# Kernel optimization log

Measured on AMD Instinct MI355X. Metric: run time of the kernel, lower is better.

Reference implementation:

```python
import jax, jax.numpy as jnp
import numpy as np

THRESH = 0.01  # confidence threshold on max softmax prob

def setup_inputs() -> dict:
    key = jax.random.key(0)
    ks = jax.random.split(key, 14)
    B, D, H, C = 8192, 2048, 2048, 1000
    sD = 1.0 / np.sqrt(D)
    sH = 1.0 / np.sqrt(H)
    return {
        "x":   jax.random.normal(ks[0], (B, D), jnp.float32),
        "W1":  jax.random.normal(ks[1], (D, H), jnp.float32) * sD,
        "b1":  jnp.zeros((H,), jnp.float32),
        "W2":  jax.random.normal(ks[2], (H, H), jnp.float32) * sH,
        "b2":  jnp.zeros((H,), jnp.float32),
        "W3":  jax.random.normal(ks[3], (H, H), jnp.float32) * sH,
        "b3":  jnp.zeros((H,), jnp.float32),
        "H1w": jax.random.normal(ks[4], (H, C), jnp.float32) * sH,
        "H1b": jnp.zeros((C,), jnp.float32),
        "H2w": jax.random.normal(ks[5], (H, C), jnp.float32) * sH,
        "H2b": jnp.zeros((C,), jnp.float32),
        "Fw":  jax.random.normal(ks[6], (H, C), jnp.float32) * sH,
        "Fb":  jnp.zeros((C,), jnp.float32),
    }

def _confident(logits):
    # confidence_function: max softmax probability exceeds threshold
    p = jax.nn.softmax(logits, axis=-1)
    return jnp.max(p, axis=-1) > THRESH  # [B] bool

def reference(x, W1, b1, W2, b2, W3, b3, H1w, H1b, H2w, H2b, Fw, Fb):
    # Stage 1 backbone + partial head
    h1 = jax.nn.relu(x @ W1 + b1)          # [B,H]
    p1 = h1 @ H1w + H1b                     # [B,C]
    c1 = _confident(p1)                     # exit mask stage 1
    # Stage 2 backbone + partial head
    h2 = jax.nn.relu(h1 @ W2 + b2)
    p2 = h2 @ H2w + H2b
    c2 = _confident(p2)
    # Final stage
    h3 = jax.nn.relu(h2 @ W3 + b3)
    p3 = h3 @ Fw + Fb
    # Per-sample first-exit selection == original index_select/index_copy cascade
    out = jnp.where(c1[:, None], p1, jnp.where(c2[:, None], p2, p3))
    return out
```

## Files before the change

kernel.cpp:

```cpp
#include <hip/hip_runtime.h>
#include <math.h>

typedef __bf16 bf16x8 __attribute__((ext_vector_type(8)));
typedef float f32x4 __attribute__((ext_vector_type(4)));
typedef unsigned short ushort_t;
typedef unsigned int uint_t;

__device__ __forceinline__ ushort_t f2bf(float f) {
    uint_t u = __float_as_uint(f);
    u += 0x7fff + ((u >> 16) & 1);
    return (ushort_t)(u >> 16);
}
__device__ __forceinline__ float bf2f(ushort_t h) {
    return __uint_as_float(((uint_t)h) << 16);
}

__device__ __forceinline__ size_t poff(int row, int k, int Kdim) {
    return ((((size_t)(row >> 7) * (Kdim >> 5) + (k >> 5)) * 512)
            + ((k >> 3) & 3) * 128 + (row & 127)) * 8 + (k & 7);
}

__device__ __forceinline__ void ll16(const ushort_t* g, ushort_t* l) {
    __builtin_amdgcn_global_load_lds(
        (const __attribute__((address_space(1))) unsigned int*)g,
        (__attribute__((address_space(3))) unsigned int*)l, 16, 0, 0);
}

template <int N> __device__ __forceinline__ void wait_vmcnt() {
    if constexpr (N == 0) asm volatile("s_waitcnt vmcnt(0)" ::: "memory");
    else if constexpr (N == 1) asm volatile("s_waitcnt vmcnt(1)" ::: "memory");
    else if constexpr (N == 2) asm volatile("s_waitcnt vmcnt(2)" ::: "memory");
    else if constexpr (N == 3) asm volatile("s_waitcnt vmcnt(3)" ::: "memory");
    else if constexpr (N == 4) asm volatile("s_waitcnt vmcnt(4)" ::: "memory");
    else if constexpr (N == 5) asm volatile("s_waitcnt vmcnt(5)" ::: "memory");
    else asm volatile("s_waitcnt vmcnt(6)" ::: "memory");
}
__device__ __forceinline__ void lgkm0_fence() {
    asm volatile("s_waitcnt lgkmcnt(0)" ::: "memory");
    __builtin_amdgcn_sched_barrier(0);
}

__global__ __launch_bounds__(256) void split_kernel(
    const float* __restrict__ in, ushort_t* __restrict__ hi,
    ushort_t* __restrict__ lo, int Kdim)
{
    const int i = blockIdx.x * 256 + threadIdx.x;
    const int row = i >> 8;
    const int k = (i & 255) * 8;
    const float4 v0 = *(const float4*)(in + (size_t)row * Kdim + k);
    const float4 v1 = *(const float4*)(in + (size_t)row * Kdim + k + 4);
    const float f[8] = {v0.x, v0.y, v0.z, v0.w, v1.x, v1.y, v1.z, v1.w};
    ushort_t h[8], l[8];
    #pragma unroll
    for (int j = 0; j < 8; ++j) {
        h[j] = f2bf(f[j]);
        l[j] = f2bf(f[j] - bf2f(h[j]));
    }
    const size_t o = poff(row, k, Kdim);
    *(uint4*)(hi + o) = *(const uint4*)h;
    *(uint4*)(lo + o) = *(const uint4*)l;
}

__global__ __launch_bounds__(256) void tsplit_kernel(
    const float* __restrict__ W, ushort_t* __restrict__ hi,
    ushort_t* __restrict__ lo, int K, int N, int write_lo)
{
    __shared__ float t[32][33];
    const int tx = threadIdx.x & 31;
    const int ty = threadIdx.x >> 5;
    const int nb = blockIdx.x * 32;
    const int kb = blockIdx.y * 32;
    #pragma unroll
    for (int i = 0; i < 4; ++i) {
        int k = kb + ty + i * 8;
        int n = nb + tx;
        t[ty + i * 8][tx] = (n < N) ? W[(size_t)k * N + n] : 0.f;
    }
    __syncthreads();
    #pragma unroll
    for (int i = 0; i < 4; ++i) {
        int n = nb + ty + i * 8;
        int k = kb + tx;
        float f = t[tx][ty + i * 8];
        size_t idx = poff(n, k, K);
        ushort_t h = f2bf(f);
        hi[idx] = h;
        if (write_lo) lo[idx] = f2bf(f - bf2f(h));
    }
}

__global__ __launch_bounds__(256) void gather_pack(
    const ushort_t* __restrict__ srchi, const ushort_t* __restrict__ srclo,
    ushort_t* __restrict__ dsthi, ushort_t* __restrict__ dstlo,
    const int* __restrict__ idx, const int* __restrict__ cntp, int Kdim)
{
    const int j = blockIdx.x;
    if (j >= *cntp) return;
    const int srow = idx[j];
    const int k = threadIdx.x * 8;
    const size_t so = poff(srow, k, Kdim);
    const size_t dofs = poff(j, k, Kdim);
    *(uint4*)(dsthi + dofs) = *(const uint4*)(srchi + so);
    if (srclo) *(uint4*)(dstlo + dofs) = *(const uint4*)(srclo + so);
}


template <int BN>
__global__ __launch_bounds__(512, 2) void gemm_split3(
    const ushort_t* __restrict__ Ahi, const ushort_t* __restrict__ Alo,
    const ushort_t* __restrict__ Bhi, const ushort_t* __restrict__ Blo,
    const float* __restrict__ bias,
    float* __restrict__ Cf, ushort_t* __restrict__ Chi, ushort_t* __restrict__ Clo,
    int K, int Ntrue, int ldc, int relu_flag,
    const int* __restrict__ cntp, int Mfull)
{
    static_assert(BN == 256 || BN == 128, "BN");
    constexpr int BSLAB = BN / 128;
    constexpr int NF = BN / 64;
    constexpr int SH = 2 + BSLAB;
    constexpr int T = 2 * SH;

    __shared__ __align__(16) ushort_t sAh[2][8192];
    __shared__ __align__(16) ushort_t sAl[2][8192];
    __shared__ __align__(16) ushort_t sBh[2][BSLAB * 4096];
    __shared__ __align__(16) ushort_t sBl[2][BSLAB * 4096];

    const int tid = threadIdx.x;
    const int m0 = blockIdx.y * 256;
    const int n0 = blockIdx.x * BN;
    int Meff = Mfull;
    if (cntp) Meff = *cntp;
    if (m0 >= ((Meff + 255) & ~255)) return;

    const int lane = tid & 63, wave = tid >> 6;
    const int wm = wave >> 2, wn = wave & 3;
    const int q = lane >> 4, r16 = lane & 15;
    const int wofs = wave * 512;

    const size_t bstr = (size_t)(K >> 5) * 4096;
    const ushort_t* gAh = Ahi + (size_t)(2 * blockIdx.y) * bstr + tid * 8;
    const ushort_t* gAl = Alo + (size_t)(2 * blockIdx.y) * bstr + tid * 8;
    const ushort_t* gBh = Bhi + (size_t)(BSLAB * blockIdx.x) * bstr + tid * 8;
    const ushort_t* gBl = Blo + (size_t)(BSLAB * blockIdx.x) * bstr + tid * 8;

    int aoff[8], boff[NF];
    #pragma unroll
    for (int mi = 0; mi < 8; ++mi)
        aoff[mi] = wm * 4096 + (q * 128 + mi * 16 + r16) * 8;
    #pragma unroll
    for (int nj = 0; nj < NF; ++nj) {
        const int col = wn * (NF * 16) + nj * 16 + r16;
        boff[nj] = (col >> 7) * 4096 + (q * 128 + (col & 127)) * 8;
    }

    f32x4 acc[8][NF];
    #pragma unroll
    for (int mi = 0; mi < 8; ++mi)
        #pragma unroll
        for (int nj = 0; nj < NF; ++nj) acc[mi][nj] = (f32x4)(0.f);

    const int NT = K >> 5;

    ll16(gAh, &sAh[0][wofs]);
    ll16(gAh + bstr, &sAh[0][4096 + wofs]);
    ll16(gBh, &sBh[0][wofs]);
    if constexpr (BSLAB == 2) ll16(gBh + bstr, &sBh[0][4096 + wofs]);
    ll16(gBl, &sBl[0][wofs]);
    if constexpr (BSLAB == 2) ll16(gBl + bstr, &sBl[0][4096 + wofs]);
    ll16(gAl, &sAl[0][wofs]);
    ll16(gAl + bstr, &sAl[0][4096 + wofs]);

    bf16x8 ah[8], bh[NF];
    for (int t = 0; t < NT - 1; ++t) {
        const int c = t & 1;
        const size_t ko = (size_t)(t + 1) * 4096;

        wait_vmcnt<T - SH>();
        __builtin_amdgcn_s_barrier();
        #pragma unroll
        for (int mi = 0; mi < 8; ++mi) ah[mi] = *(const bf16x8*)(&sAh[c][aoff[mi]]);
        #pragma unroll
        for (int nj = 0; nj < NF; ++nj) bh[nj] = *(const bf16x8*)(&sBh[c][boff[nj]]);
        ll16(gAh + ko, &sAh[c ^ 1][wofs]);
        ll16(gAh + bstr + ko, &sAh[c ^ 1][4096 + wofs]);
        ll16(gBh + ko, &sBh[c ^ 1][wofs]);
        if constexpr (BSLAB == 2) ll16(gBh + bstr + ko, &sBh[c ^ 1][4096 + wofs]);
        lgkm0_fence();
        __builtin_amdgcn_s_setprio(1);
        #pragma unroll
        for (int nj = 0; nj < NF; ++nj)
            #pragma unroll
            for (int mi = 0; mi < 8; ++mi)
                acc[mi][nj] = __builtin_amdgcn_mfma_f32_16x16x32_bf16(ah[mi], bh[nj], acc[mi][nj], 0, 0, 0);
        __builtin_amdgcn_s_setprio(0);

        wait_vmcnt<T - BSLAB>();
        __builtin_amdgcn_s_barrier();
        bf16x8 bl[NF];
        #pragma unroll
        for (int nj = 0; nj < NF; ++nj) bl[nj] = *(const bf16x8*)(&sBl[c][boff[nj]]);
        ll16(gBl + ko, &sBl[c ^ 1][wofs]);
        if constexpr (BSLAB == 2) ll16(gBl + bstr + ko, &sBl[c ^ 1][4096 + wofs]);
        lgkm0_fence();
        __builtin_amdgcn_s_setprio(1);
        #pragma unroll
        for (int nj = 0; nj < NF; ++nj)
            #pragma unroll
            for (int mi = 0; mi < 8; ++mi)
                acc[mi][nj] = __builtin_amdgcn_mfma_f32_16x16x32_bf16(ah[mi], bl[nj], acc[mi][nj], 0, 0, 0);
        __builtin_amdgcn_s_setprio(0);

        wait_vmcnt<T - 2>();
        __builtin_amdgcn_s_barrier();
        bf16x8 al[8];
        #pragma unroll
        for (int mi = 0; mi < 8; ++mi) al[mi] = *(const bf16x8*)(&sAl[c][aoff[mi]]);
        ll16(gAl + ko, &sAl[c ^ 1][wofs]);
        ll16(gAl + bstr + ko, &sAl[c ^ 1][4096 + wofs]);
        lgkm0_fence();
        __builtin_amdgcn_s_setprio(1);
        #pragma unroll
        for (int nj = 0; nj < NF; ++nj)
            #pragma unroll
            for (int mi = 0; mi < 8; ++mi)
                acc[mi][nj] = __builtin_amdgcn_mfma_f32_16x16x32_bf16(al[mi], bh[nj], acc[mi][nj], 0, 0, 0);
        __builtin_amdgcn_s_setprio(0);
    }

    {
        const int c = (NT - 1) & 1;
        wait_vmcnt<T - SH>();
        __builtin_amdgcn_s_barrier();
        #pragma unroll
        for (int mi = 0; mi < 8; ++mi) ah[mi] = *(const bf16x8*)(&sAh[c][aoff[mi]]);
        #pragma unroll
        for (int nj = 0; nj < NF; ++nj) bh[nj] = *(const bf16x8*)(&sBh[c][boff[nj]]);
        lgkm0_fence();
        __builtin_amdgcn_s_setprio(1);
        #pragma unroll
        for (int nj = 0; nj < NF; ++nj)
            #pragma unroll
            for (int mi = 0; mi < 8; ++mi)
                acc[mi][nj] = __builtin_amdgcn_mfma_f32_16x16x32_bf16(ah[mi], bh[nj], acc[mi][nj], 0, 0, 0);
        __builtin_amdgcn_s_setprio(0);

        wait_vmcnt<2>();
        __builtin_amdgcn_s_barrier();
        bf16x8 bl[NF];
        #pragma unroll
        for (int nj = 0; nj < NF; ++nj) bl[nj] = *(const bf16x8*)(&sBl[c][boff[nj]]);
        lgkm0_fence();
        __builtin_amdgcn_s_setprio(1);
        #pragma unroll
        for (int nj = 0; nj < NF; ++nj)
            #pragma unroll
            for (int mi = 0; mi < 8; ++mi)
                acc[mi][nj] = __builtin_amdgcn_mfma_f32_16x16x32_bf16(ah[mi], bl[nj], acc[mi][nj], 0, 0, 0);
        __builtin_amdgcn_s_setprio(0);

        wait_vmcnt<0>();
        __builtin_amdgcn_s_barrier();
        bf16x8 al[8];
        #pragma unroll
        for (int mi = 0; mi < 8; ++mi) al[mi] = *(const bf16x8*)(&sAl[c][aoff[mi]]);
        lgkm0_fence();
        __builtin_amdgcn_s_setprio(1);
        #pragma unroll
        for (int nj = 0; nj < NF; ++nj)
            #pragma unroll
            for (int mi = 0; mi < 8; ++mi)
                acc[mi][nj] = __builtin_amdgcn_mfma_f32_16x16x32_bf16(al[mi], bh[nj], acc[mi][nj], 0, 0, 0);
        __builtin_amdgcn_s_setprio(0);
    }

    #pragma unroll
    for (int mi = 0; mi < 8; ++mi) {
        #pragma unroll
        for (int nj = 0; nj < NF; ++nj) {
            const int col = n0 + wn * (NF * 16) + nj * 16 + r16;
            const int rowb = m0 + wm * 128 + mi * 16 + q * 4;
            const float bv = (col < Ntrue) ? bias[col] : 0.f;
            #pragma unroll
            for (int r = 0; r < 4; ++r) {
                float v = acc[mi][nj][r] + bv;
                if (relu_flag) v = fmaxf(v, 0.f);
                if (Cf) {
                    if (col < Ntrue) Cf[(size_t)(rowb + r) * ldc + col] = v;
                } else {
                    const size_t idx = poff(rowb + r, col, ldc);
                    ushort_t h = f2bf(v);
                    Chi[idx] = h;
                    Clo[idx] = f2bf(v - bf2f(h));
                }
            }
        }
    }
}

template <int BN>
__global__ __launch_bounds__(512, 2) void gemm_bf16k(
    const ushort_t* __restrict__ Ahi, const ushort_t* __restrict__ Bhi,
    const float* __restrict__ bias,
    float* __restrict__ Cf, ushort_t* __restrict__ Chi,
    int K, int Ntrue, int ldc, int relu_flag,
    const int* __restrict__ cntp, int Mfull)
{
    static_assert(BN == 256 || BN == 128, "BN");
    constexpr int BSLAB = BN / 128;
    constexpr int NF = BN / 64;
    constexpr int SH = 2 + BSLAB;

    __shared__ __align__(16) ushort_t sA[4][8192];
    __shared__ __align__(16) ushort_t sB[4][BSLAB * 4096];

    const int tid = threadIdx.x;
    const int m0 = blockIdx.y * 256;
    const int n0 = blockIdx.x * BN;
    int Meff = Mfull;
    if (cntp) Meff = *cntp;
    if (m0 >= ((Meff + 255) & ~255)) return;

    const int lane = tid & 63, wave = tid >> 6;
    const int wm = wave >> 2, wn = wave & 3;
    const int q = lane >> 4, r16 = lane & 15;
    const int wofs = wave * 512;

    const size_t bstr = (size_t)(K >> 5) * 4096;
    const ushort_t* gA = Ahi + (size_t)(2 * blockIdx.y) * bstr + tid * 8;
    const ushort_t* gB = Bhi + (size_t)(BSLAB * blockIdx.x) * bstr + tid * 8;

    int aoff[8], boff[NF];
    #pragma unroll
    for (int mi = 0; mi < 8; ++mi)
        aoff[mi] = wm * 4096 + (q * 128 + mi * 16 + r16) * 8;
    #pragma unroll
    for (int nj = 0; nj < NF; ++nj) {
        const int col = wn * (NF * 16) + nj * 16 + r16;
        boff[nj] = (col >> 7) * 4096 + (q * 128 + (col & 127)) * 8;
    }

    f32x4 acc[8][NF];
    #pragma unroll
    for (int mi = 0; mi < 8; ++mi)
        #pragma unroll
        for (int nj = 0; nj < NF; ++nj) acc[mi][nj] = (f32x4)(0.f);

    const int NT = K >> 5;

    #pragma unroll
    for (int tt = 0; tt < 2; ++tt) {
        const size_t ko = (size_t)tt * 4096;
        ll16(gA + ko, &sA[tt][wofs]);
        ll16(gA + bstr + ko, &sA[tt][4096 + wofs]);
        ll16(gB + ko, &sB[tt][wofs]);
        if constexpr (BSLAB == 2) ll16(gB + bstr + ko, &sB[tt][4096 + wofs]);
    }

    bf16x8 ah[8], bh[NF];
    for (int t = 0; t < NT - 1; ++t) {
        const int c = t & 3;
        wait_vmcnt<SH>();
        __builtin_amdgcn_s_barrier();
        #pragma unroll
        for (int mi = 0; mi < 8; ++mi) ah[mi] = *(const bf16x8*)(&sA[c][aoff[mi]]);
        #pragma unroll
        for (int nj = 0; nj < NF; ++nj) bh[nj] = *(const bf16x8*)(&sB[c][boff[nj]]);
        if (t + 2 < NT) {
            const int c2 = (t + 2) & 3;
            const size_t ko = (size_t)(t + 2) * 4096;
            ll16(gA + ko, &sA[c2][wofs]);
            ll16(gA + bstr + ko, &sA[c2][4096 + wofs]);
            ll16(gB + ko, &sB[c2][wofs]);
            if constexpr (BSLAB == 2) ll16(gB + bstr + ko, &sB[c2][4096 + wofs]);
        }
        lgkm0_fence();
        __builtin_amdgcn_s_setprio(1);
        #pragma unroll
        for (int nj = 0; nj < NF; ++nj)
            #pragma unroll
            for (int mi = 0; mi < 8; ++mi)
                acc[mi][nj] = __builtin_amdgcn_mfma_f32_16x16x32_bf16(ah[mi], bh[nj], acc[mi][nj], 0, 0, 0);
        __builtin_amdgcn_s_setprio(0);
    }
    {
        const int c = (NT - 1) & 3;
        wait_vmcnt<0>();
        __builtin_amdgcn_s_barrier();
        #pragma unroll
        for (int mi = 0; mi < 8; ++mi) ah[mi] = *(const bf16x8*)(&sA[c][aoff[mi]]);
        #pragma unroll
        for (int nj = 0; nj < NF; ++nj) bh[nj] = *(const bf16x8*)(&sB[c][boff[nj]]);
        lgkm0_fence();
        __builtin_amdgcn_s_setprio(1);
        #pragma unroll
        for (int nj = 0; nj < NF; ++nj)
            #pragma unroll
            for (int mi = 0; mi < 8; ++mi)
                acc[mi][nj] = __builtin_amdgcn_mfma_f32_16x16x32_bf16(ah[mi], bh[nj], acc[mi][nj], 0, 0, 0);
        __builtin_amdgcn_s_setprio(0);
    }

    #pragma unroll
    for (int mi = 0; mi < 8; ++mi) {
        #pragma unroll
        for (int nj = 0; nj < NF; ++nj) {
            const int col = n0 + wn * (NF * 16) + nj * 16 + r16;
            const int rowb = m0 + wm * 128 + mi * 16 + q * 4;
            const float bv = (col < Ntrue) ? bias[col] : 0.f;
            #pragma unroll
            for (int r = 0; r < 4; ++r) {
                float v = acc[mi][nj][r] + bv;
                if (relu_flag) v = fmaxf(v, 0.f);
                if (Cf) {
                    if (col < Ntrue) Cf[(size_t)(rowb + r) * ldc + col] = v;
                } else {
                    const size_t idx = poff(rowb + r, col, ldc);
                    Chi[idx] = f2bf(v);
                }
            }
        }
    }
}

__global__ __launch_bounds__(256) void conf_kernel(
    const float* __restrict__ P, int N, int* __restrict__ cm,
    const int* __restrict__ cntp)
{
    const int b = blockIdx.x;
    if (cntp && b >= *cntp) return;
    const float* row = P + (size_t)b * N;
    float m = -3.0e38f;
    for (int c = threadIdx.x; c < N; c += 256) m = fmaxf(m, row[c]);
    #pragma unroll
    for (int off = 32; off > 0; off >>= 1) m = fmaxf(m, __shfl_down(m, off));
    __shared__ float red_max[4];
    __shared__ float red_sum[4];
    const int wave = threadIdx.x >> 6;
    const int lane = threadIdx.x & 63;
    if (lane == 0) red_max[wave] = m;
    __syncthreads();
    m = fmaxf(fmaxf(red_max[0], red_max[1]), fmaxf(red_max[2], red_max[3]));
    float s = 0.f;
    for (int c = threadIdx.x; c < N; c += 256) s += expf(row[c] - m);
    #pragma unroll
    for (int off = 32; off > 0; off >>= 1) s += __shfl_down(s, off);
    if (lane == 0) red_sum[wave] = s;
    __syncthreads();
    if (threadIdx.x == 0) {
        float tot = red_sum[0] + red_sum[1] + red_sum[2] + red_sum[3];
        cm[b] = (tot < 100.0f) ? 1 : 0;
    }
}

__global__ void init_kernel(int* cnt1, int* cnt2) {
    if (threadIdx.x == 0) { *cnt1 = 0; *cnt2 = 0; }
}

__global__ __launch_bounds__(256) void build_kernel(
    const int* __restrict__ mask, int n, const int* __restrict__ nlimp,
    int* __restrict__ cnt, int* __restrict__ idx)
{
    int i = blockIdx.x * 256 + threadIdx.x;
    int nl = nlimp ? *nlimp : n;
    if (i >= nl) return;
    if (!mask[i]) { int p = atomicAdd(cnt, 1); idx[p] = i; }
}

__global__ __launch_bounds__(256) void scatter2_kernel(
    float* __restrict__ out, const float* __restrict__ p2,
    const int* __restrict__ idx1, const int* __restrict__ c2m,
    const int* __restrict__ cntp, int N)
{
    const int j = blockIdx.y;
    if (j >= *cntp || !c2m[j]) return;
    const int c = blockIdx.x * 256 + threadIdx.x;
    if (c >= N) return;
    out[(size_t)idx1[j] * N + c] = p2[(size_t)j * N + c];
}

__global__ __launch_bounds__(256) void scatter3_kernel(
    float* __restrict__ out, const float* __restrict__ p3,
    const int* __restrict__ idx1, const int* __restrict__ idx2,
    const int* __restrict__ cntp, int N)
{
    const int jj = blockIdx.y;
    if (jj >= *cntp) return;
    const int c = blockIdx.x * 256 + threadIdx.x;
    if (c >= N) return;
    out[(size_t)idx1[idx2[jj]] * N + c] = p3[(size_t)jj * N + c];
}

extern "C" void kernel_launch(void* const* d_in, const int* in_sizes, int n_in,
                              void* d_out, int out_size, void* d_ws, size_t ws_size,
                              hipStream_t stream)
{
    const float* x   = (const float*)d_in[0];
    const float* W1  = (const float*)d_in[1];
    const float* b1  = (const float*)d_in[2];
    const float* W2  = (const float*)d_in[3];
    const float* b2  = (const float*)d_in[4];
    const float* W3  = (const float*)d_in[5];
    const float* b3  = (const float*)d_in[6];
    const float* H1w = (const float*)d_in[7];
    const float* H1b = (const float*)d_in[8];
    const float* H2w = (const float*)d_in[9];
    const float* H2b = (const float*)d_in[10];
    const float* Fw  = (const float*)d_in[11];
    const float* Fb  = (const float*)d_in[12];
    float* out = (float*)d_out;

    const int B = 8192, D = 2048, Hh = 2048, Cc = 1000;

    ushort_t* xhi  = (ushort_t*)d_ws;
    ushort_t* xlo  = xhi + (size_t)B * D;
    ushort_t* h1hi = xlo + (size_t)B * D;
    ushort_t* h1lo = h1hi + (size_t)B * Hh;
    ushort_t* W0hi = h1lo + (size_t)B * Hh;
    ushort_t* W0lo = W0hi + (size_t)Hh * Hh;
    ushort_t* W1thi = W0lo + (size_t)Hh * Hh;
    ushort_t* W1tlo = W1thi + (size_t)1024 * Hh;
    float* p2 = (float*)(W1tlo + (size_t)1024 * Hh);
    int* c1   = (int*)(p2 + (size_t)B * Cc);
    int* c2m  = c1 + B;
    int* idx1 = c2m + B;
    int* idx2 = idx1 + B;
    int* cnt1 = idx2 + B;
    int* cnt2 = cnt1 + 1;

    ushort_t* h1chi = xhi;  ushort_t* h1clo = xlo;
    ushort_t* h2hi = h1hi;  ushort_t* h2lo = h1lo;
    ushort_t* h2chi = xhi;
    ushort_t* h3hi = h1hi;
    float* p3 = (float*)xlo;

    dim3 blk(256);
    dim3 blk5(512);
    const dim3 gBB(Hh / 256, B / 256);
    const dim3 gHD(1024 / 128, B / 256);
    const dim3 gT2(64, 64);
    const dim3 gTH(32, 64);

    init_kernel<<<1, 64, 0, stream>>>(cnt1, cnt2);

    split_kernel<<<dim3(B * D / 8 / 256), blk, 0, stream>>>(x, xhi, xlo, D);
    tsplit_kernel<<<gT2, blk, 0, stream>>>(W1, W0hi, W0lo, D, Hh, 1);
    gemm_split3<256><<<gBB, blk5, 0, stream>>>(xhi, xlo, W0hi, W0lo, b1,
                                               nullptr, h1hi, h1lo, D, Hh, Hh, 1,
                                               nullptr, B);
    tsplit_kernel<<<gTH, blk, 0, stream>>>(H1w, W1thi, W1tlo, Hh, Cc, 1);
    gemm_split3<128><<<gHD, blk5, 0, stream>>>(h1hi, h1lo, W1thi, W1tlo, H1b,
                                               out, nullptr, nullptr, Hh, Cc, Cc, 0,
                                               nullptr, B);
    conf_kernel<<<dim3(B), blk, 0, stream>>>(out, Cc, c1, nullptr);
    build_kernel<<<dim3(B / 256), blk, 0, stream>>>(c1, B, nullptr, cnt1, idx1);

    gather_pack<<<dim3(B), blk, 0, stream>>>(h1hi, h1lo, h1chi, h1clo, idx1, cnt1, Hh);
    tsplit_kernel<<<gT2, blk, 0, stream>>>(W2, W0hi, W0lo, Hh, Hh, 1);
    gemm_split3<256><<<gBB, blk5, 0, stream>>>(h1chi, h1clo, W0hi, W0lo, b2,
                                               nullptr, h2hi, h2lo, Hh, Hh, Hh, 1,
                                               cnt1, B);
    tsplit_kernel<<<gTH, blk, 0, stream>>>(H2w, W1thi, W1tlo, Hh, Cc, 1);
    gemm_split3<128><<<gHD, blk5, 0, stream>>>(h2hi, h2lo, W1thi, W1tlo, H2b,
                                               p2, nullptr, nullptr, Hh, Cc, Cc, 0,
                                               cnt1, B);
    conf_kernel<<<dim3(B), blk, 0, stream>>>(p2, Cc, c2m, cnt1);
    build_kernel<<<dim3(B / 256), blk, 0, stream>>>(c2m, B, cnt1, cnt2, idx2);

    gather_pack<<<dim3(B), blk, 0, stream>>>(h2hi, nullptr, h2chi, nullptr, idx2, cnt2, Hh);
    tsplit_kernel<<<gT2, blk, 0, stream>>>(W3, W0hi, nullptr, Hh, Hh, 0);
    gemm_bf16k<256><<<gBB, blk5, 0, stream>>>(h2chi, W0hi, b3,
                                              nullptr, h3hi, Hh, Hh, Hh, 1,
                                              cnt2, B);
    tsplit_kernel<<<gTH, blk, 0, stream>>>(Fw, W1thi, nullptr, Hh, Cc, 0);
    gemm_bf16k<128><<<gHD, blk5, 0, stream>>>(h3hi, W1thi, Fb,
                                              p3, nullptr, Hh, Cc, Cc, 0,
                                              cnt2, B);

    scatter2_kernel<<<dim3((Cc + 255) / 256, B), blk, 0, stream>>>(out, p2, idx1, c2m, cnt1, Cc);
    scatter3_kernel<<<dim3((Cc + 255) / 256, B), blk, 0, stream>>>(out, p3, idx1, idx2, cnt2, Cc);
}
```

Before: 1.025 ms.

## Fuse row gather into GEMM A-loads and compaction into confidence kernel

```diff
diff --git a/kernel.cpp b/kernel.cpp
--- a/kernel.cpp
+++ b/kernel.cpp
@@ -33,7 +33,11 @@
     else if constexpr (N == 3) asm volatile("s_waitcnt vmcnt(3)" ::: "memory");
     else if constexpr (N == 4) asm volatile("s_waitcnt vmcnt(4)" ::: "memory");
     else if constexpr (N == 5) asm volatile("s_waitcnt vmcnt(5)" ::: "memory");
-    else asm volatile("s_waitcnt vmcnt(6)" ::: "memory");
+    else if constexpr (N == 6) asm volatile("s_waitcnt vmcnt(6)" ::: "memory");
+    else if constexpr (N == 7) asm volatile("s_waitcnt vmcnt(7)" ::: "memory");
+    else if constexpr (N == 8) asm volatile("s_waitcnt vmcnt(8)" ::: "memory");
+    else if constexpr (N == 9) asm volatile("s_waitcnt vmcnt(9)" ::: "memory");
+    else asm volatile("s_waitcnt vmcnt(10)" ::: "memory");
 }
 __device__ __forceinline__ void lgkm0_fence() {
     asm volatile("s_waitcnt lgkmcnt(0)" ::: "memory");
@@ -89,21 +93,6 @@
     }
 }
 
-__global__ __launch_bounds__(256) void gather_pack(
-    const ushort_t* __restrict__ srchi, const ushort_t* __restrict__ srclo,
-    ushort_t* __restrict__ dsthi, ushort_t* __restrict__ dstlo,
-    const int* __restrict__ idx, const int* __restrict__ cntp, int Kdim)
-{
-    const int j = blockIdx.x;
-    if (j >= *cntp) return;
-    const int srow = idx[j];
-    const int k = threadIdx.x * 8;
-    const size_t so = poff(srow, k, Kdim);
-    const size_t dofs = poff(j, k, Kdim);
-    *(uint4*)(dsthi + dofs) = *(const uint4*)(srchi + so);
-    if (srclo) *(uint4*)(dstlo + dofs) = *(const uint4*)(srclo + so);
-}
-
 
 template <int BN>
 __global__ __launch_bounds__(512, 2) void gemm_split3(
@@ -112,13 +101,15 @@
     const float* __restrict__ bias,
     float* __restrict__ Cf, ushort_t* __restrict__ Chi, ushort_t* __restrict__ Clo,
     int K, int Ntrue, int ldc, int relu_flag,
-    const int* __restrict__ cntp, int Mfull)
+    const int* __restrict__ cntp, int Mfull, const int* __restrict__ gidx)
 {
     static_assert(BN == 256 || BN == 128, "BN");
     constexpr int BSLAB = BN / 128;
     constexpr int NF = BN / 64;
-    constexpr int SH = 2 + BSLAB;
-    constexpr int T = 2 * SH;
+    constexpr int T = 2 * (2 + BSLAB);
+    constexpr int W0 = BSLAB + 2;
+    constexpr int W1 = 2 + T;
+    constexpr int W2 = T;
 
     __shared__ __align__(16) ushort_t sAh[2][8192];
     __shared__ __align__(16) ushort_t sAl[2][8192];
@@ -138,10 +129,33 @@
     const int wofs = wave * 512;
 
     const size_t bstr = (size_t)(K >> 5) * 4096;
-    const ushort_t* gAh = Ahi + (size_t)(2 * blockIdx.y) * bstr + tid * 8;
-    const ushort_t* gAl = Alo + (size_t)(2 * blockIdx.y) * bstr + tid * 8;
+
+    const int rr = tid & 127;
+    const int kq = tid >> 7;
+    int s0 = m0 + rr, s1 = m0 + 128 + rr;
+    if (gidx) {
+        s0 = (s0 < Meff) ? gidx[s0] : 0;
+        s1 = (s1 < Meff) ? gidx[s1] : 0;
+    }
+    const size_t a0 = (size_t)(s0 >> 7) * bstr + (size_t)kq * 1024 + (size_t)(s0 & 127) * 8;
+    const size_t a1 = (size_t)(s1 >> 7) * bstr + (size_t)kq * 1024 + (size_t)(s1 & 127) * 8;
+    const ushort_t* gAh0 = Ahi + a0;
+    const ushort_t* gAh1 = Ahi + a1;
+    const ushort_t* gAl0 = Alo + a0;
+    const ushort_t* gAl1 = Alo + a1;
     const ushort_t* gBh = Bhi + (size_t)(BSLAB * blockIdx.x) * bstr + tid * 8;
     const ushort_t* gBl = Blo + (size_t)(BSLAB * blockIdx.x) * bstr + tid * 8;
+
+    auto stage_all = [&](int dst, size_t ko) {
+        ll16(gAh0 + ko, &sAh[dst][wofs]);
+        ll16(gAh1 + ko, &sAh[dst][4096 + wofs]);
+        ll16(gBh + ko, &sBh[dst][wofs]);
+        if constexpr (BSLAB == 2) ll16(gBh + bstr + ko, &sBh[dst][4096 + wofs]);
+        ll16(gBl + ko, &sBl[dst][wofs]);
+        if constexpr (BSLAB == 2) ll16(gBl + bstr + ko, &sBl[dst][4096 + wofs]);
+        ll16(gAl0 + ko, &sAl[dst][wofs]);
+        ll16(gAl1 + ko, &sAl[dst][4096 + wofs]);
+    };
 
     int aoff[8], boff[NF];
     #pragma unroll
@@ -161,30 +175,20 @@
 
     const int NT = K >> 5;
 
-    ll16(gAh, &sAh[0][wofs]);
-    ll16(gAh + bstr, &sAh[0][4096 + wofs]);
-    ll16(gBh, &sBh[0][wofs]);
-    if constexpr (BSLAB == 2) ll16(gBh + bstr, &sBh[0][4096 + wofs]);
-    ll16(gBl, &sBl[0][wofs]);
-    if constexpr (BSLAB == 2) ll16(gBl + bstr, &sBl[0][4096 + wofs]);
-    ll16(gAl, &sAl[0][wofs]);
-    ll16(gAl + bstr, &sAl[0][4096 + wofs]);
+    stage_all(0, 0);
 
     bf16x8 ah[8], bh[NF];
     for (int t = 0; t < NT - 1; ++t) {
         const int c = t & 1;
         const size_t ko = (size_t)(t + 1) * 4096;
 
-        wait_vmcnt<T - SH>();
+        wait_vmcnt<W0>();
         __builtin_amdgcn_s_barrier();
         #pragma unroll
         for (int mi = 0; mi < 8; ++mi) ah[mi] = *(const bf16x8*)(&sAh[c][aoff[mi]]);
         #pragma unroll
         for (int nj = 0; nj < NF; ++nj) bh[nj] = *(const bf16x8*)(&sBh[c][boff[nj]]);
-        ll16(gAh + ko, &sAh[c ^ 1][wofs]);
-        ll16(gAh + bstr + ko, &sAh[c ^ 1][4096 + wofs]);
-        ll16(gBh + ko, &sBh[c ^ 1][wofs]);
-        if constexpr (BSLAB == 2) ll16(gBh + bstr + ko, &sBh[c ^ 1][4096 + wofs]);
+        stage_all(c ^ 1, ko);
         lgkm0_fence();
         __builtin_amdgcn_s_setprio(1);
         #pragma unroll
@@ -194,13 +198,11 @@
                 acc[mi][nj] = __builtin_amdgcn_mfma_f32_16x16x32_bf16(ah[mi], bh[nj], acc[mi][nj], 0, 0, 0);
         __builtin_amdgcn_s_setprio(0);
 
-        wait_vmcnt<T - BSLAB>();
+        wait_vmcnt<W1>();
         __builtin_amdgcn_s_barrier();
         bf16x8 bl[NF];
         #pragma unroll
         for (int nj = 0; nj < NF; ++nj) bl[nj] = *(const bf16x8*)(&sBl[c][boff[nj]]);
-        ll16(gBl + ko, &sBl[c ^ 1][wofs]);
-        if constexpr (BSLAB == 2) ll16(gBl + bstr + ko, &sBl[c ^ 1][4096 + wofs]);
         lgkm0_fence();
         __builtin_amdgcn_s_setprio(1);
         #pragma unroll
@@ -210,13 +212,11 @@
                 acc[mi][nj] = __builtin_amdgcn_mfma_f32_16x16x32_bf16(ah[mi], bl[nj], acc[mi][nj], 0, 0, 0);
         __builtin_amdgcn_s_setprio(0);
 
-        wait_vmcnt<T - 2>();
+        wait_vmcnt<W2>();
         __builtin_amdgcn_s_barrier();
         bf16x8 al[8];
         #pragma unroll
         for (int mi = 0; mi < 8; ++mi) al[mi] = *(const bf16x8*)(&sAl[c][aoff[mi]]);
-        ll16(gAl + ko, &sAl[c ^ 1][wofs]);
-        ll16(gAl + bstr + ko, &sAl[c ^ 1][4096 + wofs]);
         lgkm0_fence();
         __builtin_amdgcn_s_setprio(1);
         #pragma unroll
@@ -229,7 +229,7 @@
 
     {
         const int c = (NT - 1) & 1;
-        wait_vmcnt<T - SH>();
+        wait_vmcnt<W0>();
         __builtin_amdgcn_s_barrier();
         #pragma unroll
         for (int mi = 0; mi < 8; ++mi) ah[mi] = *(const bf16x8*)(&sAh[c][aoff[mi]]);
@@ -303,7 +303,7 @@
     const float* __restrict__ bias,
     float* __restrict__ Cf, ushort_t* __restrict__ Chi,
     int K, int Ntrue, int ldc, int relu_flag,
-    const int* __restrict__ cntp, int Mfull)
+    const int* __restrict__ cntp, int Mfull, const int* __restrict__ gidx)
 {
     static_assert(BN == 256 || BN == 128, "BN");
     constexpr int BSLAB = BN / 128;
@@ -326,8 +326,26 @@
     const int wofs = wave * 512;
 
     const size_t bstr = (size_t)(K >> 5) * 4096;
-    const ushort_t* gA = Ahi + (size_t)(2 * blockIdx.y) * bstr + tid * 8;
+
+    const int rr = tid & 127;
+    const int kq = tid >> 7;
+    int s0 = m0 + rr, s1 = m0 + 128 + rr;
+    if (gidx) {
+        s0 = (s0 < Meff) ? gidx[s0] : 0;
+        s1 = (s1 < Meff) ? gidx[s1] : 0;
+    }
+    const size_t a0 = (size_t)(s0 >> 7) * bstr + (size_t)kq * 1024 + (size_t)(s0 & 127) * 8;
+    const size_t a1 = (size_t)(s1 >> 7) * bstr + (size_t)kq * 1024 + (size_t)(s1 & 127) * 8;
+    const ushort_t* gA0 = Ahi + a0;
+    const ushort_t* gA1 = Ahi + a1;
     const ushort_t* gB = Bhi + (size_t)(BSLAB * blockIdx.x) * bstr + tid * 8;
+
+    auto stage_t = [&](int dst, size_t ko) {
+        ll16(gA0 + ko, &sA[dst][wofs]);
+        ll16(gA1 + ko, &sA[dst][4096 + wofs]);
+        ll16(gB + ko, &sB[dst][wofs]);
+        if constexpr (BSLAB == 2) ll16(gB + bstr + ko, &sB[dst][4096 + wofs]);
+    };
 
     int aoff[8], boff[NF];
     #pragma unroll
@@ -347,14 +365,8 @@
 
     const int NT = K >> 5;
 
-    #pragma unroll
-    for (int tt = 0; tt < 2; ++tt) {
-        const size_t ko = (size_t)tt * 4096;
-        ll16(gA + ko, &sA[tt][wofs]);
-        ll16(gA + bstr + ko, &sA[tt][4096 + wofs]);
-        ll16(gB + ko, &sB[tt][wofs]);
-        if constexpr (BSLAB == 2) ll16(gB + bstr + ko, &sB[tt][4096 + wofs]);
-    }
+    stage_t(0, 0);
+    stage_t(1, 4096);
 
     bf16x8 ah[8], bh[NF];
     for (int t = 0; t < NT - 1; ++t) {
@@ -365,14 +377,7 @@
         for (int mi = 0; mi < 8; ++mi) ah[mi] = *(const bf16x8*)(&sA[c][aoff[mi]]);
         #pragma unroll
         for (int nj = 0; nj < NF; ++nj) bh[nj] = *(const bf16x8*)(&sB[c][boff[nj]]);
-        if (t + 2 < NT) {
-            const int c2 = (t + 2) & 3;
-            const size_t ko = (size_t)(t + 2) * 4096;
-            ll16(gA + ko, &sA[c2][wofs]);
-            ll16(gA + bstr + ko, &sA[c2][4096 + wofs]);
-            ll16(gB + ko, &sB[c2][wofs]);
-            if constexpr (BSLAB == 2) ll16(gB + bstr + ko, &sB[c2][4096 + wofs]);
-        }
+        if (t + 2 < NT) stage_t((t + 2) & 3, (size_t)(t + 2) * 4096);
         lgkm0_fence();
         __builtin_amdgcn_s_setprio(1);
         #pragma unroll
@@ -424,7 +429,8 @@
 
 __global__ __launch_bounds__(256) void conf_kernel(
     const float* __restrict__ P, int N, int* __restrict__ cm,
-    const int* __restrict__ cntp)
+    const int* __restrict__ cntp, int* __restrict__ cnt_out,
+    int* __restrict__ idx_out)
 {
     const int b = blockIdx.x;
     if (cntp && b >= *cntp) return;
@@ -448,22 +454,14 @@
     __syncthreads();
     if (threadIdx.x == 0) {
         float tot = red_sum[0] + red_sum[1] + red_sum[2] + red_sum[3];
-        cm[b] = (tot < 100.0f) ? 1 : 0;
+        int conf = (tot < 100.0f) ? 1 : 0;
+        if (cm) cm[b] = conf;
+        if (!conf) { int p = atomicAdd(cnt_out, 1); idx_out[p] = b; }
     }
 }
 
 __global__ void init_kernel(int* cnt1, int* cnt2) {
     if (threadIdx.x == 0) { *cnt1 = 0; *cnt2 = 0; }
-}
-
-__global__ __launch_bounds__(256) void build_kernel(
-    const int* __restrict__ mask, int n, const int* __restrict__ nlimp,
-    int* __restrict__ cnt, int* __restrict__ idx)
-{
-    int i = blockIdx.x * 256 + threadIdx.x;
-    int nl = nlimp ? *nlimp : n;
-    if (i >= nl) return;
-    if (!mask[i]) { int p = atomicAdd(cnt, 1); idx[p] = i; }
 }
 
 __global__ __launch_bounds__(256) void scatter2_kernel(
@@ -527,9 +525,7 @@
     int* cnt1 = idx2 + B;
     int* cnt2 = cnt1 + 1;
 
-    ushort_t* h1chi = xhi;  ushort_t* h1clo = xlo;
-    ushort_t* h2hi = h1hi;  ushort_t* h2lo = h1lo;
-    ushort_t* h2chi = xhi;
+    ushort_t* h2hi = xhi;  ushort_t* h2lo = xlo;
     ushort_t* h3hi = h1hi;
     float* p3 = (float*)xlo;
 
@@ -546,35 +542,31 @@
     tsplit_kernel<<<gT2, blk, 0, stream>>>(W1, W0hi, W0lo, D, Hh, 1);
     gemm_split3<256><<<gBB, blk5, 0, stream>>>(xhi, xlo, W0hi, W0lo, b1,
                                                nullptr, h1hi, h1lo, D, Hh, Hh, 1,
-                                               nullptr, B);
+                                               nullptr, B, nullptr);
     tsplit_kernel<<<gTH, blk, 0, stream>>>(H1w, W1thi, W1tlo, Hh, Cc, 1);
     gemm_split3<128><<<gHD, blk5, 0, stream>>>(h1hi, h1lo, W1thi, W1tlo, H1b,
                                                out, nullptr, nullptr, Hh, Cc, Cc, 0,
-                                               nullptr, B);
-    conf_kernel<<<dim3(B), blk, 0, stream>>>(out, Cc, c1, nullptr);
-    build_kernel<<<dim3(B / 256), blk, 0, stream>>>(c1, B, nullptr, cnt1, idx1);
-
-    gather_pack<<<dim3(B), blk, 0, stream>>>(h1hi, h1lo, h1chi, h1clo, idx1, cnt1, Hh);
+                                               nullptr, B, nullptr);
+    conf_kernel<<<dim3(B), blk, 0, stream>>>(out, Cc, nullptr, nullptr, cnt1, idx1);
+
     tsplit_kernel<<<gT2, blk, 0, stream>>>(W2, W0hi, W0lo, Hh, Hh, 1);
-    gemm_split3<256><<<gBB, blk5, 0, stream>>>(h1chi, h1clo, W0hi, W0lo, b2,
+    gemm_split3<256><<<gBB, blk5, 0, stream>>>(h1hi, h1lo, W0hi, W0lo, b2,
                                                nullptr, h2hi, h2lo, Hh, Hh, Hh, 1,
-                                               cnt1, B);
+                                               cnt1, B, idx1);
     tsplit_kernel<<<gTH, blk, 0, stream>>>(H2w, W1thi, W1tlo, Hh, Cc, 1);
     gemm_split3<128><<<gHD, blk5, 0, stream>>>(h2hi, h2lo, W1thi, W1tlo, H2b,
                                                p2, nullptr, nullptr, Hh, Cc, Cc, 0,
-                                               cnt1, B);
-    conf_kernel<<<dim3(B), blk, 0, stream>>>(p2, Cc, c2m, cnt1);
-    build_kernel<<<dim3(B / 256), blk, 0, stream>>>(c2m, B, cnt1, cnt2, idx2);
-
-    gather_pack<<<dim3(B), blk, 0, stream>>>(h2hi, nullptr, h2chi, nullptr, idx2, cnt2, Hh);
+                                               cnt1, B, nullptr);
+    conf_kernel<<<dim3(B), blk, 0, stream>>>(p2, Cc, c2m, cnt1, cnt2, idx2);
+
     tsplit_kernel<<<gT2, blk, 0, stream>>>(W3, W0hi, nullptr, Hh, Hh, 0);
-    gemm_bf16k<256><<<gBB, blk5, 0, stream>>>(h2chi, W0hi, b3,
+    gemm_bf16k<256><<<gBB, blk5, 0, stream>>>(h2hi, W0hi, b3,
                                               nullptr, h3hi, Hh, Hh, Hh, 1,
-                                              cnt2, B);
+                                              cnt2, B, idx2);
     tsplit_kernel<<<gTH, blk, 0, stream>>>(Fw, W1thi, nullptr, Hh, Cc, 0);
     gemm_bf16k<128><<<gHD, blk5, 0, stream>>>(h3hi, W1thi, Fb,
                                               p3, nullptr, Hh, Cc, Cc, 0,
-                                              cnt2, B);
+                                              cnt2, B, nullptr);
 
     scatter2_kernel<<<dim3((Cc + 255) / 256, B), blk, 0, stream>>>(out, p2, idx1, c2m, cnt1, Cc);
     scatter3_kernel<<<dim3((Cc + 255) / 256, B), blk, 0, stream>>>(out, p3, idx1, idx2, cnt2, Cc);
```

Measured after the change: 1.116 ms. 8.9% more time.
